# Kernel optimization log

Measured on AMD Instinct MI355X. Metric: run time of the kernel, lower is better.

The kernel has to match this reference:

```python
import jax, jax.numpy as jnp
import numpy as np

EPS = 1e-5
B, S, D = 4, 2048, 128
BALL_SCALE = 0.05  # keeps points inside the unit Poincare ball for c=1


def setup_inputs() -> dict:
    key = jax.random.key(0)
    kq, kk, kv = jax.random.split(key, 3)
    q = jax.random.normal(kq, (B, S, D), dtype=jnp.float32) * BALL_SCALE
    k = jax.random.normal(kk, (B, S, D), dtype=jnp.float32) * BALL_SCALE
    v_tangent = jax.random.normal(kv, (B, S, D), dtype=jnp.float32)
    c = jnp.asarray(1.0, dtype=jnp.float32)
    beta = jnp.asarray(0.0, dtype=jnp.float32)            # nn.Parameter init 0.0
    attention_bias = jnp.asarray(0.0, dtype=jnp.float32)  # nn.Parameter init 0.0
    return {"q": q, "k": k, "v_tangent": v_tangent, "c": c,
            "beta": beta, "attention_bias": attention_bias}


def reference(q, k, v_tangent, c, beta, attention_bias):
    sqrt_c = jnp.sqrt(c)

    # --- pairwise Poincare distance (all fp32, as in the torch autocast block) ---
    x_norm_sq = jnp.sum(q * q, axis=-1, keepdims=True)            # (B,S,1)
    y_norm_sq = jnp.sum(k * k, axis=-1, keepdims=True)            # (B,S,1)
    xy_dot = jnp.einsum('bsd,btd->bst', q, k)                     # (B,S,S)
    y_norm_sq_t = jnp.swapaxes(y_norm_sq, -2, -1)                 # (B,1,S)
    diff_norm_sq = x_norm_sq - 2.0 * xy_dot + y_norm_sq_t         # ||x-y||^2, (B,S,S)
    denom = (1.0 - c * x_norm_sq) * (1.0 - c * y_norm_sq_t)       # (B,S,S)
    arg = 1.0 + 2.0 * c * diff_norm_sq / jnp.maximum(denom, EPS)
    dist = jnp.arccosh(jnp.maximum(arg, 1.0 + EPS)) / sqrt_c      # (B,S,S)

    # --- attention ---
    beta_positive = jax.nn.softplus(beta)
    attention_scores = -beta_positive * dist - attention_bias
    attention_weights = jax.nn.softmax(attention_scores, axis=-1)  # (B,S,S)
    output_tangent = jnp.einsum('bst,btd->bsd', attention_weights, v_tangent)

    # --- exp map at origin ---
    v_norm = jnp.maximum(
        jnp.sqrt(jnp.sum(output_tangent * output_tangent, axis=-1, keepdims=True)), EPS)
    output_hyperbolic = (jnp.tanh(sqrt_c * v_norm) / sqrt_c) * (output_tangent / v_norm)

    return output_hyperbolic, attention_weights
```

## Files before the change

kernel.cpp:

```cpp
#include <hip/hip_runtime.h>
#include <math.h>

#define B_ 4
#define S_ 2048
#define D_ 128
#define EPSF 1e-5f
#define BN 128
#define PSB 272
#define PRS 4128

typedef __attribute__((ext_vector_type(8))) short short8;
typedef __attribute__((ext_vector_type(4))) float f32x4;

static __device__ __forceinline__ unsigned short f2bf(float f) {
    unsigned u = __float_as_uint(f);
    return (unsigned short)((u + 0x7fffu + ((u >> 16) & 1u)) >> 16);
}


__global__ __launch_bounds__(256) void convqk_kernel(const float* __restrict__ q,
                                                     const float* __restrict__ k,
                                                     const float* __restrict__ cp,
                                                     float* __restrict__ qn, float* __restrict__ kn,
                                                     float* __restrict__ lws,
                                                     float2* __restrict__ qng, float2* __restrict__ kng,
                                                     unsigned* __restrict__ Qb, unsigned* __restrict__ Kb) {
    int row = blockIdx.x * 4 + (threadIdx.x >> 6);
    int lane = threadIdx.x & 63;
    const int NR = B_ * S_;
    const float cc = cp[0];
    bool isQ = row < NR;
    int r = isQ ? row : row - NR;
    float2 v = ((const float2*)(isQ ? q : k))[(size_t)r * 64 + lane];
    unsigned pk = (unsigned)f2bf(v.x) | ((unsigned)f2bf(v.y) << 16);
    float nrm = v.x * v.x + v.y * v.y;
#pragma unroll
    for (int m = 1; m <= 32; m <<= 1) nrm += __shfl_xor(nrm, m, 64);
    if (isQ) {
        Qb[(size_t)r * 64 + lane] = pk;
        if (lane == 0) {
            qn[r] = nrm;
            qng[r] = make_float2(nrm, 2.f * cc * __builtin_amdgcn_rcpf(1.f - cc * nrm));
        }
        if (lane == 1) lws[r] = 0.f;
    } else {
        int b = r >> 11, rbk = r & 2047;
        int tile = rbk >> 7, n = rbk & 127;
        Kb[(size_t)b * 131072 + tile * 8192 + (lane >> 4) * 2048 + n * 16 +
           ((lane >> 2) & 3) * 4 + (lane & 3)] = pk;
        if (lane == 0) {
            kn[r] = nrm;
            kng[r] = make_float2(nrm, __builtin_amdgcn_rcpf(1.f - cc * nrm));
        }
    }
}

__global__ __launch_bounds__(256) void convv_kernel(const float* __restrict__ v, uint4* __restrict__ Vtb) {
    __shared__ unsigned short Vs[128 * 132];
    int b = blockIdx.x >> 4;
    int t = blockIdx.x & 15;
    int tid = threadIdx.x;
    const float* src = v + ((size_t)b * S_ + t * 128) * D_;
    int d4 = tid & 31, key0 = tid >> 5;
#pragma unroll
    for (int it = 0; it < 16; ++it) {
        int key = key0 + it * 8;
        float4 f = *(const float4*)(src + (size_t)key * D_ + d4 * 4);
        unsigned short* dst = &Vs[key * 132 + d4 * 4];
        dst[0] = f2bf(f.x); dst[1] = f2bf(f.y); dst[2] = f2bf(f.z); dst[3] = f2bf(f.w);
    }
    __syncthreads();
    uint4* tile = Vtb + (size_t)blockIdx.x * (128 * 16);
    int d = tid & 127;
    int cl = tid >> 7;
#pragma unroll
    for (int it = 0; it < 8; ++it) {
        int c = cl + it * 2;
        int kb = c * 8;
        unsigned short e0 = Vs[(kb + 0) * 132 + d], e1 = Vs[(kb + 1) * 132 + d];
        unsigned short e2 = Vs[(kb + 2) * 132 + d], e3 = Vs[(kb + 3) * 132 + d];
        unsigned short e4 = Vs[(kb + 4) * 132 + d], e5 = Vs[(kb + 5) * 132 + d];
        unsigned short e6 = Vs[(kb + 6) * 132 + d], e7 = Vs[(kb + 7) * 132 + d];
        uint4 o;
        o.x = (unsigned)e0 | ((unsigned)e1 << 16);
        o.y = (unsigned)e2 | ((unsigned)e3 << 16);
        o.z = (unsigned)e4 | ((unsigned)e5 << 16);
        o.w = (unsigned)e6 | ((unsigned)e7 << 16);
        tile[(c >> 2) * 512 + d * 4 + (c & 3)] = o;
    }
}


__global__ __launch_bounds__(512, 4) void hattn8_kernel(
    const unsigned short* __restrict__ Qb, const char* __restrict__ Kb, const char* __restrict__ Vtb,
    const float2* __restrict__ qng, const float2* __restrict__ kng,
    const float* __restrict__ cp, const float* __restrict__ betap, const float* __restrict__ biasp,
    float* __restrict__ hout, float* __restrict__ wout) {

    __shared__ __align__(1024) char smem[66304];
    float* l_row = (float*)(smem + 66176);
    float* nsq_s = (float*)(smem + 66240);

    const int tid = threadIdx.x;
    const int lane = tid & 63, wave = tid >> 6;
    const int wn = wave;
    const int lm = lane & 15, quad = lane >> 4;

    int xcd = blockIdx.x & 7;
    int b = xcd >> 1;
    int rb = (blockIdx.x >> 3) * 2 + (xcd & 1);
    int s0 = rb * 16;
    const size_t bS = (size_t)b * S_;

    const float beta = betap[0], bias = biasp[0];
    const float cc = cp[0];
    const float beta_pos = fmaxf(beta, 0.f) + log1pf(__expf(-fabsf(beta)));
    const float sqrt_c = sqrtf(cc);
    const float bneg = -beta_pos / sqrt_c;
    const float bias2 = -bias * 1.442695040888963f;
    const float onepe = 1.f + EPSF;

    const char* KbBase = Kb + (size_t)b * 524288;
    const char* VtBase = Vtb + (size_t)b * 16 * 32768;

    if (tid < 16) {
        float2 x = qng[bS + s0 + tid];
        *(float2*)(smem + 66048 + tid * 8) = x;
    } else if (tid < 32) {
        l_row[tid - 16] = 0.f;
    } else if (tid < 48) {
        nsq_s[tid - 32] = 0.f;
    }

    const int n0 = wn * 16 + lm;
    const int foff = n0 * 64 + quad * 16;
    short8 kf[4];
    float2 yg;
    {
#pragma unroll
        for (int ks = 0; ks < 4; ++ks)
            kf[ks] = *(const short8*)(KbBase + ks * 8192 + foff);
        yg = kng[bS + n0];
    }

    short8 aq[4];
    {
        const unsigned short* qrow = Qb + (bS + s0 + lm) * D_;
#pragma unroll
        for (int ks = 0; ks < 4; ++ks)
            aq[ks] = *(const short8*)(qrow + ks * 32 + quad * 8);
    }

    __syncthreads();

    float2 xr4[4];
#pragma unroll
    for (int r = 0; r < 4; ++r)
        xr4[r] = *(const float2*)(smem + 66048 + (quad * 4 + r) * 8);

    f32x4 o = {0.f, 0.f, 0.f, 0.f};
    float lacc[4] = {0.f, 0.f, 0.f, 0.f};

    for (int it = 0; it < 16; ++it) {
        short8 kfn[4], vf[4];
        float2 ygn;
        {
            const char* vb = VtBase + (size_t)it * 32768 + foff;
#pragma unroll
            for (int ks = 0; ks < 4; ++ks)
                vf[ks] = *(const short8*)(vb + ks * 8192);
        }
        if (it < 15) {
            const char* kb = KbBase + (size_t)(it + 1) * 32768 + foff;
#pragma unroll
            for (int ks = 0; ks < 4; ++ks)
                kfn[ks] = *(const short8*)(kb + ks * 8192);
            ygn = kng[bS + (size_t)(it + 1) * 128 + n0];
        }
        __builtin_amdgcn_sched_barrier(0);

        f32x4 acc = {0.f, 0.f, 0.f, 0.f};
#pragma unroll
        for (int ks = 0; ks < 4; ++ks)
            acc = __builtin_amdgcn_mfma_f32_16x16x32_bf16(aq[ks], kf[ks], acc, 0, 0, 0);

#pragma unroll
        for (int r = 0; r < 4; ++r) {
            int row = quad * 4 + r;
            float diff = fmaf(-2.f, acc[r], xr4[r].x + yg.x);
            float arg = fmaf(diff * yg.y, xr4[r].y, 1.f);
            arg = fmaxf(arg, onepe);
            float w = arg + sqrtf(fmaf(arg, arg, -1.f));
            float pv = __builtin_amdgcn_exp2f(fmaf(bneg, __builtin_amdgcn_logf(w), bias2));
            *(unsigned short*)(smem + row * PRS + (it * 128 + n0) * 2) = f2bf(pv);
            lacc[r] += pv;
        }
        __syncthreads();

        {
            const char* prow = smem + lm * PRS + it * 256 + quad * 16;
#pragma unroll
            for (int ks = 0; ks < 4; ++ks) {
                short8 ap = *(const short8*)(prow + ks * 64);
                o = __builtin_amdgcn_mfma_f32_16x16x32_bf16(ap, vf[ks], o, 0, 0, 0);
            }
        }

        if (it < 15) {
#pragma unroll
            for (int ks = 0; ks < 4; ++ks) kf[ks] = kfn[ks];
            yg = ygn;
        }
    }

#pragma unroll
    for (int r = 0; r < 4; ++r) {
        float s = lacc[r];
#pragma unroll
        for (int m = 1; m <= 8; m <<= 1) s += __shfl_xor(s, m, 64);
        if (lm == 0) atomicAdd(&l_row[quad * 4 + r], s);
    }
    __syncthreads();

    float linv[4];
#pragma unroll
    for (int r = 0; r < 4; ++r) linv[r] = 1.f / l_row[quad * 4 + r];

#pragma unroll
    for (int r = 0; r < 4; ++r) {
        float x = o[r] * linv[r];
        o[r] = x;
        float np = x * x;
#pragma unroll
        for (int m = 1; m <= 8; m <<= 1) np += __shfl_xor(np, m, 64);
        if (lm == 0) atomicAdd(&nsq_s[quad * 4 + r], np);
    }
    __syncthreads();
#pragma unroll
    for (int r = 0; r < 4; ++r) {
        int row = quad * 4 + r;
        float vn = fmaxf(sqrtf(nsq_s[row]), EPSF);
        float a = sqrt_c * vn;
        float th = 1.f - 2.f / (__expf(2.f * a) + 1.f);
        float sc = th / a;
        hout[(bS + s0 + row) * D_ + n0] = o[r] * sc;
    }

    {
        float4* wdst = (float4*)(wout + (bS + s0) * (size_t)S_);
#pragma unroll
        for (int j = 0; j < 8; ++j) {
            int idx = tid + j * 512;
            int row = idx >> 8;
            int ch = idx & 255;
            float lr = 1.f / l_row[row];
            uint4 u = *(const uint4*)(smem + row * PRS + ch * 16);
            float4 f0, f1;
            f0.x = __uint_as_float(u.x << 16) * lr;
            f0.y = __uint_as_float(u.x & 0xffff0000u) * lr;
            f0.z = __uint_as_float(u.y << 16) * lr;
            f0.w = __uint_as_float(u.y & 0xffff0000u) * lr;
            f1.x = __uint_as_float(u.z << 16) * lr;
            f1.y = __uint_as_float(u.z & 0xffff0000u) * lr;
            f1.z = __uint_as_float(u.w << 16) * lr;
            f1.w = __uint_as_float(u.w & 0xffff0000u) * lr;
            wdst[idx * 2] = f0;
            wdst[idx * 2 + 1] = f1;
        }
    }
}


__global__ __launch_bounds__(512, 2) void hattn_kernel(
    const unsigned short* __restrict__ Qb, const char* __restrict__ Kb, const char* __restrict__ Vtb,
    const float* __restrict__ qn, const float* __restrict__ kn,
    const float* __restrict__ cp, const float* __restrict__ betap, const float* __restrict__ biasp,
    float* __restrict__ lws, float* __restrict__ houtg, float* __restrict__ woutg) {

    __shared__ __align__(1024) char smem[75136];
    char* KsB = smem;
    char* VtB = smem + 32768;
    char* PsB = smem + 65536;
    float* kn_s  = (float*)(smem + 74240);
    float* qn_s  = (float*)(smem + 74752);
    float* l_row = (float*)(smem + 74880);
    float* nsq_s = (float*)(smem + 75008);

    const int tid = threadIdx.x;
    const int lane = tid & 63, wave = tid >> 6;
    const int wm = wave & 1, wn = wave >> 1;
    const int lm = lane & 15, quad = lane >> 4;

    int xcd = blockIdx.x & 7;
    int b = xcd >> 1;
    int rb = (blockIdx.x >> 3) * 2 + (xcd & 1);
    int s0 = rb * 32;
    const size_t bS = (size_t)b * S_;

    const float cc = cp[0], beta = betap[0], bias = biasp[0];
    const float beta_pos = fmaxf(beta, 0.f) + log1pf(__expf(-fabsf(beta)));
    const float sqrt_c = sqrtf(cc);
    const float inv_sqrt_c = 1.f / sqrt_c;

    if (tid < 32) {
        qn_s[tid] = qn[bS + s0 + tid];
        l_row[tid] = 0.f;
        nsq_s[tid] = 0.f;
    }

    short8 aq[4];
    {
        const unsigned short* qrow = Qb + (bS + s0 + wm * 16 + lm) * D_;
#pragma unroll
        for (int ks = 0; ks < 4; ++ks)
            aq[ks] = *(const short8*)(qrow + ks * 32 + quad * 8);
    }

    f32x4 o0 = {0.f, 0.f, 0.f, 0.f}, o1 = {0.f, 0.f, 0.f, 0.f};

    const char* KbBase = Kb + (size_t)b * 524288;
    const char* VtBase = Vtb + (size_t)b * 16 * 32768;

    for (int t = 0; t < S_ / BN; ++t) {
        int t0 = t * BN;
        __syncthreads();
        {
            const uint4* ksrc = (const uint4*)(KbBase + (size_t)t * 32768);
            const uint4* vsrc = (const uint4*)(VtBase + (size_t)t * 32768);
            uint4* kd = (uint4*)KsB;
            uint4* vd = (uint4*)VtB;
#pragma unroll
            for (int i = 0; i < 4; ++i) {
                kd[tid + i * 512] = ksrc[tid + i * 512];
                vd[tid + i * 512] = vsrc[tid + i * 512];
            }
            if (tid < BN) kn_s[tid] = kn[bS + t0 + tid];
        }
        __syncthreads();

        int n0 = wn * 32 + lm;
        f32x4 acc0 = {0.f, 0.f, 0.f, 0.f}, acc1 = {0.f, 0.f, 0.f, 0.f};
#pragma unroll
        for (int ks = 0; ks < 4; ++ks) {
            short8 b0 = *(const short8*)(KsB + ks * 8192 + n0 * 64 + quad * 16);
            short8 b1 = *(const short8*)(KsB + ks * 8192 + (n0 + 16) * 64 + quad * 16);
            acc0 = __builtin_amdgcn_mfma_f32_16x16x32_bf16(aq[ks], b0, acc0, 0, 0, 0);
            acc1 = __builtin_amdgcn_mfma_f32_16x16x32_bf16(aq[ks], b1, acc1, 0, 0, 0);
        }

        float lp[4];
#pragma unroll
        for (int r = 0; r < 4; ++r) {
            int row = wm * 16 + quad * 4 + r;
            float xn = qn_s[row];
            float fx = 1.f - cc * xn;
            float p0, p1;
#pragma unroll
            for (int nt = 0; nt < 2; ++nt) {
                int col = wn * 32 + nt * 16 + lm;
                float dot = (nt == 0) ? acc0[r] : acc1[r];
                float yn = kn_s[col];
                float diff = xn - 2.f * dot + yn;
                float den = fmaxf(fx * (1.f - cc * yn), EPSF);
                float arg = fmaf(2.f * cc * diff, __builtin_amdgcn_rcpf(den), 1.f);
                arg = fmaxf(arg, 1.f + EPSF);
                float dist = __logf(arg + sqrtf(arg * arg - 1.f)) * inv_sqrt_c;
                float p = __expf(fmaf(-beta_pos, dist, -bias));
                woutg[(bS + s0 + row) * S_ + t0 + col] = p;
                *(unsigned short*)(PsB + row * PSB + col * 2) = f2bf(p);
                if (nt == 0) p0 = p; else p1 = p;
            }
            lp[r] = p0 + p1;
        }
#pragma unroll
        for (int r = 0; r < 4; ++r) {
            float s = lp[r];
#pragma unroll
            for (int m = 1; m <= 8; m <<= 1) s += __shfl_xor(s, m, 64);
            if (lm == 0) atomicAdd(&l_row[wm * 16 + quad * 4 + r], s);
        }
        __syncthreads();

#pragma unroll
        for (int ks = 0; ks < 4; ++ks) {
            short8 ap = *(const short8*)(PsB + (wm * 16 + lm) * PSB + (ks * 32 + quad * 8) * 2);
            int d0 = wn * 32 + lm;
            short8 v0 = *(const short8*)(VtB + ks * 8192 + d0 * 64 + quad * 16);
            short8 v1 = *(const short8*)(VtB + ks * 8192 + (d0 + 16) * 64 + quad * 16);
            o0 = __builtin_amdgcn_mfma_f32_16x16x32_bf16(ap, v0, o0, 0, 0, 0);
            o1 = __builtin_amdgcn_mfma_f32_16x16x32_bf16(ap, v1, o1, 0, 0, 0);
        }
    }
    __syncthreads();

    float xs0[4], xs1[4];
#pragma unroll
    for (int r = 0; r < 4; ++r) {
        int row = wm * 16 + quad * 4 + r;
        float linv = __builtin_amdgcn_rcpf(l_row[row]);
        float x0 = o0[r] * linv, x1 = o1[r] * linv;
        xs0[r] = x0; xs1[r] = x1;
        float np = x0 * x0 + x1 * x1;
#pragma unroll
        for (int m = 1; m <= 8; m <<= 1) np += __shfl_xor(np, m, 64);
        if (lm == 0) atomicAdd(&nsq_s[row], np);
    }
    if (tid < 32) lws[bS + s0 + tid] = l_row[tid];
    __syncthreads();
#pragma unroll
    for (int r = 0; r < 4; ++r) {
        int row = wm * 16 + quad * 4 + r;
        float vn = fmaxf(sqrtf(nsq_s[row]), EPSF);
        float a = sqrt_c * vn;
        float th = 1.f - 2.f * __builtin_amdgcn_rcpf(__expf(2.f * a) + 1.f);
        float sc = th / a;
        houtg[(bS + s0 + row) * D_ + wn * 32 + lm] = xs0[r] * sc;
        houtg[(bS + s0 + row) * D_ + wn * 32 + 16 + lm] = xs1[r] * sc;
    }
}

__global__ __launch_bounds__(256) void wnorm_kernel(float* __restrict__ w,
                                                    const float* __restrict__ lws) {
    size_t idx = (size_t)blockIdx.x * 256 + threadIdx.x;
    int row = (int)(idx >> 9);
    float linv = 1.f / lws[row];
    float4* p = (float4*)w + idx;
    float4 v = *p;
    v.x *= linv; v.y *= linv; v.z *= linv; v.w *= linv;
    *p = v;
}


extern "C" void kernel_launch(void* const* d_in, const int* in_sizes, int n_in,
                              void* d_out, int out_size, void* d_ws, size_t ws_size,
                              hipStream_t stream) {
    const float* q    = (const float*)d_in[0];
    const float* k    = (const float*)d_in[1];
    const float* v    = (const float*)d_in[2];
    const float* c    = (const float*)d_in[3];
    const float* beta = (const float*)d_in[4];
    const float* ab   = (const float*)d_in[5];

    float* out  = (float*)d_out;
    float* hout = out;
    float* wout = out + (size_t)B_ * S_ * D_;

    float* qn  = (float*)d_ws;
    float* kn  = qn + B_ * S_;
    float* lws = kn + B_ * S_;
    char*  wsb = (char*)d_ws;
    const size_t QG_OFF = 98304;
    const size_t KG_OFF = QG_OFF + 65536;
    const size_t QB_OFF = KG_OFF + 65536;
    const size_t KB_OFF = QB_OFF + 2097152;
    const size_t VT_OFF = KB_OFF + 2097152;
    const size_t NEED1  = VT_OFF + 2097152;

    float2*  qng = (float2*)(wsb + QG_OFF);
    float2*  kng = (float2*)(wsb + KG_OFF);
    unsigned* Qb = (unsigned*)(wsb + QB_OFF);
    unsigned* Kb = (unsigned*)(wsb + KB_OFF);
    uint4*   Vtb = (uint4*)(wsb + VT_OFF);

    if (ws_size >= NEED1) {
        convqk_kernel<<<4096, 256, 0, stream>>>(q, k, c, qn, kn, lws, qng, kng, Qb, Kb);
        convv_kernel<<<64, 256, 0, stream>>>(v, Vtb);
        hattn8_kernel<<<512, 512, 0, stream>>>((const unsigned short*)Qb, (const char*)Kb,
                                               (const char*)Vtb, qng, kng, c, beta, ab,
                                               hout, wout);
    } else {
        convqk_kernel<<<4096, 256, 0, stream>>>(q, k, c, qn, kn, lws, qng, kng, Qb, Kb);
        convv_kernel<<<64, 256, 0, stream>>>(v, Vtb);
        hattn_kernel<<<256, 512, 0, stream>>>((const unsigned short*)Qb, (const char*)Kb,
                                              (const char*)Vtb, qn, kn, c, beta, ab,
                                              lws, hout, wout);
        wnorm_kernel<<<(B_ * S_ * S_ / 4) / 256, 256, 0, stream>>>(wout, lws);
    }
}
```

Baseline: 137.8 us.

## Split keys across waves with register-shuffled P and LDS output reduction

The main attention kernel changes from each wave owning a 16-key column slice per tile, with a block-wide barrier every iteration, to each wave owning its own 32-key chunks. It computes S transposed (keys × queries) so the probabilities can be reshuffled in registers into the A operand of the PV MFMA, feeding eight output accumulators across all 128 value dims. Per-wave partial outputs are then reduced through LDS atomics before normalization and the exp map. This removes the per-iteration __syncthreads and the LDS round trip for P, but adds register pressure, cross-wave atomic reductions and extra LDS. K is now stored row-major, and the fallback kernel gains an XOR swizzle to match.

```diff
diff --git a/kernel.cpp b/kernel.cpp
--- a/kernel.cpp
+++ b/kernel.cpp
@@ -44,10 +44,7 @@
         }
         if (lane == 1) lws[r] = 0.f;
     } else {
-        int b = r >> 11, rbk = r & 2047;
-        int tile = rbk >> 7, n = rbk & 127;
-        Kb[(size_t)b * 131072 + tile * 8192 + (lane >> 4) * 2048 + n * 16 +
-           ((lane >> 2) & 3) * 4 + (lane & 3)] = pk;
+        Kb[(size_t)r * 64 + lane] = pk;
         if (lane == 0) {
             kn[r] = nrm;
             kng[r] = make_float2(nrm, __builtin_amdgcn_rcpf(1.f - cc * nrm));
@@ -91,19 +88,20 @@
 }
 
 
-__global__ __launch_bounds__(512, 4) void hattn8_kernel(
-    const unsigned short* __restrict__ Qb, const char* __restrict__ Kb, const char* __restrict__ Vtb,
+__global__ __launch_bounds__(512, 4) void hattn9_kernel(
+    const unsigned short* __restrict__ Qb, const unsigned short* __restrict__ Kb,
+    const char* __restrict__ Vtb,
     const float2* __restrict__ qng, const float2* __restrict__ kng,
     const float* __restrict__ cp, const float* __restrict__ betap, const float* __restrict__ biasp,
     float* __restrict__ hout, float* __restrict__ wout) {
 
-    __shared__ __align__(1024) char smem[66304];
-    float* l_row = (float*)(smem + 66176);
-    float* nsq_s = (float*)(smem + 66240);
+    __shared__ __align__(1024) char smem[74368];
+    float* O_red = (float*)(smem + 66048);
+    float* l_row = (float*)(smem + 74240);
+    float* nsq_s = (float*)(smem + 74304);
 
     const int tid = threadIdx.x;
-    const int lane = tid & 63, wave = tid >> 6;
-    const int wn = wave;
+    const int lane = tid & 63, wn = tid >> 6;
     const int lm = lane & 15, quad = lane >> 4;
 
     int xcd = blockIdx.x & 7;
@@ -120,28 +118,15 @@
     const float bias2 = -bias * 1.442695040888963f;
     const float onepe = 1.f + EPSF;
 
-    const char* KbBase = Kb + (size_t)b * 524288;
+    const unsigned short* KbR = Kb + bS * D_;
     const char* VtBase = Vtb + (size_t)b * 16 * 32768;
 
-    if (tid < 16) {
-        float2 x = qng[bS + s0 + tid];
-        *(float2*)(smem + 66048 + tid * 8) = x;
-    } else if (tid < 32) {
-        l_row[tid - 16] = 0.f;
-    } else if (tid < 48) {
-        nsq_s[tid - 32] = 0.f;
-    }
-
-    const int n0 = wn * 16 + lm;
-    const int foff = n0 * 64 + quad * 16;
-    short8 kf[4];
-    float2 yg;
-    {
-#pragma unroll
-        for (int ks = 0; ks < 4; ++ks)
-            kf[ks] = *(const short8*)(KbBase + ks * 8192 + foff);
-        yg = kng[bS + n0];
-    }
+#pragma unroll
+    for (int j = 0; j < 4; ++j) O_red[tid + j * 512] = 0.f;
+    if (tid < 16) l_row[tid] = 0.f;
+    else if (tid < 32) nsq_s[tid - 16] = 0.f;
+
+    const float2 xq = qng[bS + s0 + lm];
 
     short8 aq[4];
     {
@@ -150,100 +135,148 @@
         for (int ks = 0; ks < 4; ++ks)
             aq[ks] = *(const short8*)(qrow + ks * 32 + quad * 8);
     }
-
     __syncthreads();
 
-    float2 xr4[4];
-#pragma unroll
-    for (int r = 0; r < 4; ++r)
-        xr4[r] = *(const float2*)(smem + 66048 + (quad * 4 + r) * 8);
-
-    f32x4 o = {0.f, 0.f, 0.f, 0.f};
-    float lacc[4] = {0.f, 0.f, 0.f, 0.f};
-
-    for (int it = 0; it < 16; ++it) {
-        short8 kfn[4], vf[4];
-        float2 ygn;
-        {
-            const char* vb = VtBase + (size_t)it * 32768 + foff;
-#pragma unroll
-            for (int ks = 0; ks < 4; ++ks)
-                vf[ks] = *(const short8*)(vb + ks * 8192);
-        }
-        if (it < 15) {
-            const char* kb = KbBase + (size_t)(it + 1) * 32768 + foff;
-#pragma unroll
-            for (int ks = 0; ks < 4; ++ks)
-                kfn[ks] = *(const short8*)(kb + ks * 8192);
-            ygn = kng[bS + (size_t)(it + 1) * 128 + n0];
-        }
-        __builtin_amdgcn_sched_barrier(0);
-
-        f32x4 acc = {0.f, 0.f, 0.f, 0.f};
-#pragma unroll
-        for (int ks = 0; ks < 4; ++ks)
-            acc = __builtin_amdgcn_mfma_f32_16x16x32_bf16(aq[ks], kf[ks], acc, 0, 0, 0);
-
+    f32x4 o0 = {0,0,0,0}, o1 = {0,0,0,0}, o2 = {0,0,0,0}, o3 = {0,0,0,0};
+    f32x4 o4 = {0,0,0,0}, o5 = {0,0,0,0}, o6 = {0,0,0,0}, o7 = {0,0,0,0};
+    float lacc = 0.f;
+
+    const int srcA = lm + ((quad & 1) << 5);
+    const int srcB = srcA + 16;
+    const bool hiT = quad >= 2;
+
+    for (int ci = 0; ci < 8; ++ci) {
+        const int chunk = ci * 8 + wn;
+        const int key0 = chunk * 32;
+
+        const unsigned short* krow = KbR + (size_t)(key0 + lm) * D_;
+        short8 kfA[4], kfB[4];
+#pragma unroll
+        for (int ks = 0; ks < 4; ++ks) {
+            kfA[ks] = *(const short8*)(krow + ks * 32 + quad * 8);
+            kfB[ks] = *(const short8*)(krow + 16 * D_ + ks * 32 + quad * 8);
+        }
+
+        float2 ygA[4], ygB[4];
 #pragma unroll
         for (int r = 0; r < 4; ++r) {
-            int row = quad * 4 + r;
-            float diff = fmaf(-2.f, acc[r], xr4[r].x + yg.x);
-            float arg = fmaf(diff * yg.y, xr4[r].y, 1.f);
-            arg = fmaxf(arg, onepe);
+            ygA[r] = kng[bS + key0 + quad * 4 + r];
+            ygB[r] = kng[bS + key0 + 16 + quad * 4 + r];
+        }
+
+        f32x4 sA = {0,0,0,0}, sB = {0,0,0,0};
+#pragma unroll
+        for (int ks = 0; ks < 4; ++ks) {
+            sA = __builtin_amdgcn_mfma_f32_16x16x32_bf16(kfA[ks], aq[ks], sA, 0, 0, 0);
+            sB = __builtin_amdgcn_mfma_f32_16x16x32_bf16(kfB[ks], aq[ks], sB, 0, 0, 0);
+        }
+
+        unsigned short pb[8];
+#pragma unroll
+        for (int r = 0; r < 4; ++r) {
+            float diff = fmaf(-2.f, sA[r], xq.x + ygA[r].x);
+            float arg = fmaxf(fmaf(diff * ygA[r].y, xq.y, 1.f), onepe);
             float w = arg + sqrtf(fmaf(arg, arg, -1.f));
             float pv = __builtin_amdgcn_exp2f(fmaf(bneg, __builtin_amdgcn_logf(w), bias2));
-            *(unsigned short*)(smem + row * PRS + (it * 128 + n0) * 2) = f2bf(pv);
-            lacc[r] += pv;
-        }
-        __syncthreads();
+            pb[r] = f2bf(pv);
+            lacc += pv;
+
+            float diff2 = fmaf(-2.f, sB[r], xq.x + ygB[r].x);
+            float arg2 = fmaxf(fmaf(diff2 * ygB[r].y, xq.y, 1.f), onepe);
+            float w2 = arg2 + sqrtf(fmaf(arg2, arg2, -1.f));
+            float pv2 = __builtin_amdgcn_exp2f(fmaf(bneg, __builtin_amdgcn_logf(w2), bias2));
+            pb[4 + r] = f2bf(pv2);
+            lacc += pv2;
+        }
+        unsigned u0 = (unsigned)pb[0] | ((unsigned)pb[1] << 16);
+        unsigned u1 = (unsigned)pb[2] | ((unsigned)pb[3] << 16);
+        unsigned u2 = (unsigned)pb[4] | ((unsigned)pb[5] << 16);
+        unsigned u3 = (unsigned)pb[6] | ((unsigned)pb[7] << 16);
 
         {
-            const char* prow = smem + lm * PRS + it * 256 + quad * 16;
-#pragma unroll
-            for (int ks = 0; ks < 4; ++ks) {
-                short8 ap = *(const short8*)(prow + ks * 64);
-                o = __builtin_amdgcn_mfma_f32_16x16x32_bf16(ap, vf[ks], o, 0, 0, 0);
-            }
-        }
-
-        if (it < 15) {
-#pragma unroll
-            for (int ks = 0; ks < 4; ++ks) kf[ks] = kfn[ks];
-            yg = ygn;
-        }
-    }
-
-#pragma unroll
-    for (int r = 0; r < 4; ++r) {
-        float s = lacc[r];
-#pragma unroll
-        for (int m = 1; m <= 8; m <<= 1) s += __shfl_xor(s, m, 64);
-        if (lm == 0) atomicAdd(&l_row[quad * 4 + r], s);
+            char* pw = smem + lm * PRS + (key0 + quad * 4) * 2;
+            *(uint2*)pw = make_uint2(u0, u1);
+            *(uint2*)(pw + 32) = make_uint2(u2, u3);
+        }
+
+        unsigned a0, a1, a2, a3;
+        {
+            unsigned f0 = __shfl((int)u0, srcA), f1 = __shfl((int)u1, srcA);
+            unsigned f2 = __shfl((int)u0, srcB), f3 = __shfl((int)u1, srcB);
+            unsigned g0 = __shfl((int)u2, srcA), g1 = __shfl((int)u3, srcA);
+            unsigned g2 = __shfl((int)u2, srcB), g3 = __shfl((int)u3, srcB);
+            a0 = hiT ? g0 : f0; a1 = hiT ? g1 : f1;
+            a2 = hiT ? g2 : f2; a3 = hiT ? g3 : f3;
+        }
+        union { unsigned u[4]; short8 s; } pa;
+        pa.u[0] = a0; pa.u[1] = a1; pa.u[2] = a2; pa.u[3] = a3;
+
+        const char* vb = VtBase + (size_t)(chunk >> 2) * 32768 + (chunk & 3) * 8192
+                         + lm * 64 + quad * 16;
+        {
+            short8 vf;
+            vf = *(const short8*)(vb + 0 * 1024);
+            o0 = __builtin_amdgcn_mfma_f32_16x16x32_bf16(pa.s, vf, o0, 0, 0, 0);
+            vf = *(const short8*)(vb + 1 * 1024);
+            o1 = __builtin_amdgcn_mfma_f32_16x16x32_bf16(pa.s, vf, o1, 0, 0, 0);
+            vf = *(const short8*)(vb + 2 * 1024);
+            o2 = __builtin_amdgcn_mfma_f32_16x16x32_bf16(pa.s, vf, o2, 0, 0, 0);
+            vf = *(const short8*)(vb + 3 * 1024);
+            o3 = __builtin_amdgcn_mfma_f32_16x16x32_bf16(pa.s, vf, o3, 0, 0, 0);
+            vf = *(const short8*)(vb + 4 * 1024);
+            o4 = __builtin_amdgcn_mfma_f32_16x16x32_bf16(pa.s, vf, o4, 0, 0, 0);
+            vf = *(const short8*)(vb + 5 * 1024);
+            o5 = __builtin_amdgcn_mfma_f32_16x16x32_bf16(pa.s, vf, o5, 0, 0, 0);
+            vf = *(const short8*)(vb + 6 * 1024);
+            o6 = __builtin_amdgcn_mfma_f32_16x16x32_bf16(pa.s, vf, o6, 0, 0, 0);
+            vf = *(const short8*)(vb + 7 * 1024);
+            o7 = __builtin_amdgcn_mfma_f32_16x16x32_bf16(pa.s, vf, o7, 0, 0, 0);
+        }
+    }
+
+    lacc += __shfl_xor(lacc, 16, 64);
+    lacc += __shfl_xor(lacc, 32, 64);
+    if (lane < 16) atomicAdd(&l_row[lm], lacc);
+
+    {
+        float* Obase = O_red + (quad * 4) * 128 + lm;
+#pragma unroll
+        for (int r = 0; r < 4; ++r) {
+            atomicAdd(Obase + r * 128 + 0 * 16, o0[r]);
+            atomicAdd(Obase + r * 128 + 1 * 16, o1[r]);
+            atomicAdd(Obase + r * 128 + 2 * 16, o2[r]);
+            atomicAdd(Obase + r * 128 + 3 * 16, o3[r]);
+            atomicAdd(Obase + r * 128 + 4 * 16, o4[r]);
+            atomicAdd(Obase + r * 128 + 5 * 16, o5[r]);
+            atomicAdd(Obase + r * 128 + 6 * 16, o6[r]);
+            atomicAdd(Obase + r * 128 + 7 * 16, o7[r]);
+        }
     }
     __syncthreads();
 
-    float linv[4];
-#pragma unroll
-    for (int r = 0; r < 4; ++r) linv[r] = 1.f / l_row[quad * 4 + r];
-
-#pragma unroll
-    for (int r = 0; r < 4; ++r) {
-        float x = o[r] * linv[r];
-        o[r] = x;
+    float xs[4];
+#pragma unroll
+    for (int j = 0; j < 4; ++j) {
+        int idx = tid + j * 512;
+        int row = idx >> 7;
+        float x = O_red[idx] / l_row[row];
+        xs[j] = x;
         float np = x * x;
 #pragma unroll
-        for (int m = 1; m <= 8; m <<= 1) np += __shfl_xor(np, m, 64);
-        if (lm == 0) atomicAdd(&nsq_s[quad * 4 + r], np);
+        for (int m = 1; m <= 32; m <<= 1) np += __shfl_xor(np, m, 64);
+        if (lane == 0) atomicAdd(&nsq_s[row], np);
     }
     __syncthreads();
-#pragma unroll
-    for (int r = 0; r < 4; ++r) {
-        int row = quad * 4 + r;
+
+#pragma unroll
+    for (int j = 0; j < 4; ++j) {
+        int idx = tid + j * 512;
+        int row = idx >> 7;
         float vn = fmaxf(sqrtf(nsq_s[row]), EPSF);
         float a = sqrt_c * vn;
         float th = 1.f - 2.f / (__expf(2.f * a) + 1.f);
         float sc = th / a;
-        hout[(bS + s0 + row) * D_ + n0] = o[r] * sc;
+        hout[(bS + s0 + row) * D_ + (idx & 127)] = xs[j] * sc;
     }
 
     {
@@ -272,7 +305,8 @@
 
 
 __global__ __launch_bounds__(512, 2) void hattn_kernel(
-    const unsigned short* __restrict__ Qb, const char* __restrict__ Kb, const char* __restrict__ Vtb,
+    const unsigned short* __restrict__ Qb, const unsigned short* __restrict__ Kb,
+    const char* __restrict__ Vtb,
     const float* __restrict__ qn, const float* __restrict__ kn,
     const float* __restrict__ cp, const float* __restrict__ betap, const float* __restrict__ biasp,
     float* __restrict__ lws, float* __restrict__ houtg, float* __restrict__ woutg) {
@@ -318,21 +352,23 @@
 
     f32x4 o0 = {0.f, 0.f, 0.f, 0.f}, o1 = {0.f, 0.f, 0.f, 0.f};
 
-    const char* KbBase = Kb + (size_t)b * 524288;
+    const uint4* KbBase = (const uint4*)(Kb + bS * D_);
     const char* VtBase = Vtb + (size_t)b * 16 * 32768;
 
     for (int t = 0; t < S_ / BN; ++t) {
         int t0 = t * BN;
         __syncthreads();
         {
-            const uint4* ksrc = (const uint4*)(KbBase + (size_t)t * 32768);
+            const uint4* ksrc = KbBase + (size_t)t0 * 16;
             const uint4* vsrc = (const uint4*)(VtBase + (size_t)t * 32768);
             uint4* kd = (uint4*)KsB;
             uint4* vd = (uint4*)VtB;
 #pragma unroll
             for (int i = 0; i < 4; ++i) {
-                kd[tid + i * 512] = ksrc[tid + i * 512];
-                vd[tid + i * 512] = vsrc[tid + i * 512];
+                int idx = tid + i * 512;
+                int row = idx >> 4, cch = idx & 15;
+                kd[row * 16 + (cch ^ (row & 7))] = ksrc[idx];
+                vd[idx] = vsrc[idx];
             }
             if (tid < BN) kn_s[tid] = kn[bS + t0 + tid];
         }
@@ -342,8 +378,10 @@
         f32x4 acc0 = {0.f, 0.f, 0.f, 0.f}, acc1 = {0.f, 0.f, 0.f, 0.f};
 #pragma unroll
         for (int ks = 0; ks < 4; ++ks) {
-            short8 b0 = *(const short8*)(KsB + ks * 8192 + n0 * 64 + quad * 16);
-            short8 b1 = *(const short8*)(KsB + ks * 8192 + (n0 + 16) * 64 + quad * 16);
+            int c = ks * 4 + quad;
+            short8 b0 = *(const short8*)(KsB + n0 * 256 + ((c ^ (n0 & 7)) * 16));
+            int n1 = n0 + 16;
+            short8 b1 = *(const short8*)(KsB + n1 * 256 + ((c ^ (n1 & 7)) * 16));
             acc0 = __builtin_amdgcn_mfma_f32_16x16x32_bf16(aq[ks], b0, acc0, 0, 0, 0);
             acc1 = __builtin_amdgcn_mfma_f32_16x16x32_bf16(aq[ks], b1, acc1, 0, 0, 0);
         }
@@ -465,13 +503,13 @@
     if (ws_size >= NEED1) {
         convqk_kernel<<<4096, 256, 0, stream>>>(q, k, c, qn, kn, lws, qng, kng, Qb, Kb);
         convv_kernel<<<64, 256, 0, stream>>>(v, Vtb);
-        hattn8_kernel<<<512, 512, 0, stream>>>((const unsigned short*)Qb, (const char*)Kb,
+        hattn9_kernel<<<512, 512, 0, stream>>>((const unsigned short*)Qb, (const unsigned short*)Kb,
                                                (const char*)Vtb, qng, kng, c, beta, ab,
                                                hout, wout);
     } else {
         convqk_kernel<<<4096, 256, 0, stream>>>(q, k, c, qn, kn, lws, qng, kng, Qb, Kb);
         convv_kernel<<<64, 256, 0, stream>>>(v, Vtb);
-        hattn_kernel<<<256, 512, 0, stream>>>((const unsigned short*)Qb, (const char*)Kb,
+        hattn_kernel<<<256, 512, 0, stream>>>((const unsigned short*)Qb, (const unsigned short*)Kb,
                                               (const char*)Vtb, qn, kn, c, beta, ab,
                                               lws, hout, wout);
         wnorm_kernel<<<(B_ * S_ * S_ / 4) / 256, 256, 0, stream>>>(wout, lws);
```

New measurement: 190.5 us. 1.38x slower.

## Use two-pass softmax with recomputed scores to shrink LDS and stream weights

Applied to the files above, without the earlier changes.

Replaces the single-pass attention kernel, which kept a full 16x2048 bf16 probability row block in LDS, with a two-pass scheme. The first pass computes only row sums. The second pass recomputes the distance scores with the normalization folded into the exponent, then writes the normalized weights directly to global memory and uses a small double-buffered LDS tile for the PV MFMA. K gets a new transposed per-16-key layout so the score MFMA runs K-major, and the fallback kernel switches to row-major K with an XOR swizzle. The aim is far less LDS per block and higher occupancy (launch bounds raised to 6). The cost is doubling the QK matmul and transcendental work, plus an extra K layout pass in the conversion kernel.

```diff
diff --git a/kernel.cpp b/kernel.cpp
--- a/kernel.cpp
+++ b/kernel.cpp
@@ -7,7 +7,7 @@
 #define EPSF 1e-5f
 #define BN 128
 #define PSB 272
-#define PRS 4128
+#define SRS 272
 
 typedef __attribute__((ext_vector_type(8))) short short8;
 typedef __attribute__((ext_vector_type(4))) float f32x4;
@@ -24,7 +24,8 @@
                                                      float* __restrict__ qn, float* __restrict__ kn,
                                                      float* __restrict__ lws,
                                                      float2* __restrict__ qng, float2* __restrict__ kng,
-                                                     unsigned* __restrict__ Qb, unsigned* __restrict__ Kb) {
+                                                     unsigned* __restrict__ Qb, unsigned* __restrict__ Kb,
+                                                     unsigned* __restrict__ KbA) {
     int row = blockIdx.x * 4 + (threadIdx.x >> 6);
     int lane = threadIdx.x & 63;
     const int NR = B_ * S_;
@@ -44,10 +45,11 @@
         }
         if (lane == 1) lws[r] = 0.f;
     } else {
-        int b = r >> 11, rbk = r & 2047;
-        int tile = rbk >> 7, n = rbk & 127;
-        Kb[(size_t)b * 131072 + tile * 8192 + (lane >> 4) * 2048 + n * 16 +
-           ((lane >> 2) & 3) * 4 + (lane & 3)] = pk;
+        Kb[(size_t)r * 64 + lane] = pk;
+        int b = r >> 11, rloc = r & 2047;
+        int t16 = rloc >> 4, kit = rloc & 15;
+        KbA[(size_t)b * 131072 + t16 * 1024 + (lane >> 4) * 256 + kit * 16 +
+            ((lane >> 2) & 3) * 4 + (lane & 3)] = pk;
         if (lane == 0) {
             kn[r] = nrm;
             kng[r] = make_float2(nrm, __builtin_amdgcn_rcpf(1.f - cc * nrm));
@@ -91,19 +93,19 @@
 }
 
 
-__global__ __launch_bounds__(512, 4) void hattn8_kernel(
-    const unsigned short* __restrict__ Qb, const char* __restrict__ Kb, const char* __restrict__ Vtb,
+__global__ __launch_bounds__(512, 6) void hattn10_kernel(
+    const unsigned short* __restrict__ Qb, const char* __restrict__ KbA,
+    const char* __restrict__ Vtb,
     const float2* __restrict__ qng, const float2* __restrict__ kng,
     const float* __restrict__ cp, const float* __restrict__ betap, const float* __restrict__ biasp,
     float* __restrict__ hout, float* __restrict__ wout) {
 
-    __shared__ __align__(1024) char smem[66304];
-    float* l_row = (float*)(smem + 66176);
-    float* nsq_s = (float*)(smem + 66240);
+    __shared__ __align__(1024) char smem[8832];
+    float* l_row = (float*)(smem + 8704);
+    float* nsq_s = (float*)(smem + 8768);
 
     const int tid = threadIdx.x;
-    const int lane = tid & 63, wave = tid >> 6;
-    const int wn = wave;
+    const int lane = tid & 63, wn = tid >> 6;
     const int lm = lane & 15, quad = lane >> 4;
 
     int xcd = blockIdx.x & 7;
@@ -120,28 +122,13 @@
     const float bias2 = -bias * 1.442695040888963f;
     const float onepe = 1.f + EPSF;
 
-    const char* KbBase = Kb + (size_t)b * 524288;
-    const char* VtBase = Vtb + (size_t)b * 16 * 32768;
-
-    if (tid < 16) {
-        float2 x = qng[bS + s0 + tid];
-        *(float2*)(smem + 66048 + tid * 8) = x;
-    } else if (tid < 32) {
-        l_row[tid - 16] = 0.f;
-    } else if (tid < 48) {
-        nsq_s[tid - 32] = 0.f;
-    }
-
-    const int n0 = wn * 16 + lm;
-    const int foff = n0 * 64 + quad * 16;
-    short8 kf[4];
-    float2 yg;
-    {
-#pragma unroll
-        for (int ks = 0; ks < 4; ++ks)
-            kf[ks] = *(const short8*)(KbBase + ks * 8192 + foff);
-        yg = kng[bS + n0];
-    }
+    const char* KA = KbA + (size_t)b * 524288;
+    const char* Vt = Vtb + (size_t)b * 524288;
+
+    if (tid < 16) l_row[tid] = 0.f;
+    else if (tid < 32) nsq_s[tid - 16] = 0.f;
+
+    const float2 xq = qng[bS + s0 + lm];
 
     short8 aq[4];
     {
@@ -150,92 +137,107 @@
         for (int ks = 0; ks < 4; ++ks)
             aq[ks] = *(const short8*)(qrow + ks * 32 + quad * 8);
     }
-
-    __syncthreads();
-
-    float2 xr4[4];
-#pragma unroll
-    for (int r = 0; r < 4; ++r)
-        xr4[r] = *(const float2*)(smem + 66048 + (quad * 4 + r) * 8);
+    __syncthreads();
+
+    float lacc = 0.f;
+    for (int it = 0; it < 16; ++it) {
+        int t16 = it * 8 + wn;
+        const char* ka = KA + t16 * 4096 + lm * 64 + quad * 16;
+        short8 k0 = *(const short8*)(ka);
+        short8 k1 = *(const short8*)(ka + 1024);
+        short8 k2 = *(const short8*)(ka + 2048);
+        short8 k3 = *(const short8*)(ka + 3072);
+        const float4* yp = (const float4*)(kng + bS + t16 * 16 + quad * 4);
+        float4 y01 = yp[0], y23 = yp[1];
+
+        f32x4 s = {0.f, 0.f, 0.f, 0.f};
+        s = __builtin_amdgcn_mfma_f32_16x16x32_bf16(k0, aq[0], s, 0, 0, 0);
+        s = __builtin_amdgcn_mfma_f32_16x16x32_bf16(k1, aq[1], s, 0, 0, 0);
+        s = __builtin_amdgcn_mfma_f32_16x16x32_bf16(k2, aq[2], s, 0, 0, 0);
+        s = __builtin_amdgcn_mfma_f32_16x16x32_bf16(k3, aq[3], s, 0, 0, 0);
+
+        float yn[4] = {y01.x, y01.z, y23.x, y23.z};
+        float gy[4] = {y01.y, y01.w, y23.y, y23.w};
+#pragma unroll
+        for (int r = 0; r < 4; ++r) {
+            float diff = fmaf(-2.f, s[r], xq.x + yn[r]);
+            float arg = fmaxf(fmaf(diff * gy[r], xq.y, 1.f), onepe);
+            float w = arg + sqrtf(fmaf(arg, arg, -1.f));
+            lacc += __builtin_amdgcn_exp2f(fmaf(bneg, __builtin_amdgcn_logf(w), bias2));
+        }
+    }
+    lacc += __shfl_xor(lacc, 16, 64);
+    lacc += __shfl_xor(lacc, 32, 64);
+    if (lane < 16) atomicAdd(&l_row[lm], lacc);
+    __syncthreads();
+
+    const float lrow = l_row[lm];
+    const float linv = 1.f / lrow;
+    const float bias3 = bias2 - __builtin_amdgcn_logf(lrow);
 
     f32x4 o = {0.f, 0.f, 0.f, 0.f};
-    float lacc[4] = {0.f, 0.f, 0.f, 0.f};
-
+    int pbuf = 0;
     for (int it = 0; it < 16; ++it) {
-        short8 kfn[4], vf[4];
-        float2 ygn;
+        int t16 = it * 8 + wn;
+        const char* ka = KA + t16 * 4096 + lm * 64 + quad * 16;
+        short8 k0 = *(const short8*)(ka);
+        short8 k1 = *(const short8*)(ka + 1024);
+        short8 k2 = *(const short8*)(ka + 2048);
+        short8 k3 = *(const short8*)(ka + 3072);
+        const float4* yp = (const float4*)(kng + bS + t16 * 16 + quad * 4);
+        float4 y01 = yp[0], y23 = yp[1];
+
+        f32x4 s = {0.f, 0.f, 0.f, 0.f};
+        s = __builtin_amdgcn_mfma_f32_16x16x32_bf16(k0, aq[0], s, 0, 0, 0);
+        s = __builtin_amdgcn_mfma_f32_16x16x32_bf16(k1, aq[1], s, 0, 0, 0);
+        s = __builtin_amdgcn_mfma_f32_16x16x32_bf16(k2, aq[2], s, 0, 0, 0);
+        s = __builtin_amdgcn_mfma_f32_16x16x32_bf16(k3, aq[3], s, 0, 0, 0);
+
+        float yn[4] = {y01.x, y01.z, y23.x, y23.z};
+        float gy[4] = {y01.y, y01.w, y23.y, y23.w};
+        float pv[4];
+#pragma unroll
+        for (int r = 0; r < 4; ++r) {
+            float diff = fmaf(-2.f, s[r], xq.x + yn[r]);
+            float arg = fmaxf(fmaf(diff * gy[r], xq.y, 1.f), onepe);
+            float w = arg + sqrtf(fmaf(arg, arg, -1.f));
+            pv[r] = __builtin_amdgcn_exp2f(fmaf(bneg, __builtin_amdgcn_logf(w), bias3));
+        }
+
         {
-            const char* vb = VtBase + (size_t)it * 32768 + foff;
-#pragma unroll
-            for (int ks = 0; ks < 4; ++ks)
-                vf[ks] = *(const short8*)(vb + ks * 8192);
-        }
-        if (it < 15) {
-            const char* kb = KbBase + (size_t)(it + 1) * 32768 + foff;
-#pragma unroll
-            for (int ks = 0; ks < 4; ++ks)
-                kfn[ks] = *(const short8*)(kb + ks * 8192);
-            ygn = kng[bS + (size_t)(it + 1) * 128 + n0];
-        }
-        __builtin_amdgcn_sched_barrier(0);
-
-        f32x4 acc = {0.f, 0.f, 0.f, 0.f};
-#pragma unroll
-        for (int ks = 0; ks < 4; ++ks)
-            acc = __builtin_amdgcn_mfma_f32_16x16x32_bf16(aq[ks], kf[ks], acc, 0, 0, 0);
-
-#pragma unroll
-        for (int r = 0; r < 4; ++r) {
-            int row = quad * 4 + r;
-            float diff = fmaf(-2.f, acc[r], xr4[r].x + yg.x);
-            float arg = fmaf(diff * yg.y, xr4[r].y, 1.f);
-            arg = fmaxf(arg, onepe);
-            float w = arg + sqrtf(fmaf(arg, arg, -1.f));
-            float pv = __builtin_amdgcn_exp2f(fmaf(bneg, __builtin_amdgcn_logf(w), bias2));
-            *(unsigned short*)(smem + row * PRS + (it * 128 + n0) * 2) = f2bf(pv);
-            lacc[r] += pv;
+            float4 wv = {pv[0], pv[1], pv[2], pv[3]};
+            *(float4*)(wout + (bS + s0 + lm) * (size_t)S_ + t16 * 16 + quad * 4) = wv;
+        }
+
+        {
+            unsigned u0 = (unsigned)f2bf(pv[0]) | ((unsigned)f2bf(pv[1]) << 16);
+            unsigned u1 = (unsigned)f2bf(pv[2]) | ((unsigned)f2bf(pv[3]) << 16);
+            *(uint2*)(smem + pbuf * 4352 + lm * SRS + wn * 32 + quad * 8) = make_uint2(u0, u1);
         }
         __syncthreads();
 
         {
-            const char* prow = smem + lm * PRS + it * 256 + quad * 16;
-#pragma unroll
-            for (int ks = 0; ks < 4; ++ks) {
-                short8 ap = *(const short8*)(prow + ks * 64);
-                o = __builtin_amdgcn_mfma_f32_16x16x32_bf16(ap, vf[ks], o, 0, 0, 0);
+            const char* sr = smem + pbuf * 4352 + lm * SRS;
+            const char* vb = Vt + (size_t)it * 32768 + (wn * 16 + lm) * 64 + quad * 16;
+#pragma unroll
+            for (int kq = 0; kq < 4; ++kq) {
+                short8 ap = *(const short8*)(sr + kq * 64 + quad * 16);
+                short8 vf = *(const short8*)(vb + kq * 8192);
+                o = __builtin_amdgcn_mfma_f32_16x16x32_bf16(ap, vf, o, 0, 0, 0);
             }
         }
-
-        if (it < 15) {
-#pragma unroll
-            for (int ks = 0; ks < 4; ++ks) kf[ks] = kfn[ks];
-            yg = ygn;
-        }
+        pbuf ^= 1;
     }
 
 #pragma unroll
     for (int r = 0; r < 4; ++r) {
-        float s = lacc[r];
-#pragma unroll
-        for (int m = 1; m <= 8; m <<= 1) s += __shfl_xor(s, m, 64);
-        if (lm == 0) atomicAdd(&l_row[quad * 4 + r], s);
-    }
-    __syncthreads();
-
-    float linv[4];
-#pragma unroll
-    for (int r = 0; r < 4; ++r) linv[r] = 1.f / l_row[quad * 4 + r];
-
-#pragma unroll
-    for (int r = 0; r < 4; ++r) {
-        float x = o[r] * linv[r];
-        o[r] = x;
-        float np = x * x;
+        float np = o[r] * o[r];
 #pragma unroll
         for (int m = 1; m <= 8; m <<= 1) np += __shfl_xor(np, m, 64);
         if (lm == 0) atomicAdd(&nsq_s[quad * 4 + r], np);
     }
     __syncthreads();
+
 #pragma unroll
     for (int r = 0; r < 4; ++r) {
         int row = quad * 4 + r;
@@ -243,36 +245,14 @@
         float a = sqrt_c * vn;
         float th = 1.f - 2.f / (__expf(2.f * a) + 1.f);
         float sc = th / a;
-        hout[(bS + s0 + row) * D_ + n0] = o[r] * sc;
-    }
-
-    {
-        float4* wdst = (float4*)(wout + (bS + s0) * (size_t)S_);
-#pragma unroll
-        for (int j = 0; j < 8; ++j) {
-            int idx = tid + j * 512;
-            int row = idx >> 8;
-            int ch = idx & 255;
-            float lr = 1.f / l_row[row];
-            uint4 u = *(const uint4*)(smem + row * PRS + ch * 16);
-            float4 f0, f1;
-            f0.x = __uint_as_float(u.x << 16) * lr;
-            f0.y = __uint_as_float(u.x & 0xffff0000u) * lr;
-            f0.z = __uint_as_float(u.y << 16) * lr;
-            f0.w = __uint_as_float(u.y & 0xffff0000u) * lr;
-            f1.x = __uint_as_float(u.z << 16) * lr;
-            f1.y = __uint_as_float(u.z & 0xffff0000u) * lr;
-            f1.z = __uint_as_float(u.w << 16) * lr;
-            f1.w = __uint_as_float(u.w & 0xffff0000u) * lr;
-            wdst[idx * 2] = f0;
-            wdst[idx * 2 + 1] = f1;
-        }
+        hout[(bS + s0 + row) * D_ + wn * 16 + lm] = o[r] * sc;
     }
 }
 
 
 __global__ __launch_bounds__(512, 2) void hattn_kernel(
-    const unsigned short* __restrict__ Qb, const char* __restrict__ Kb, const char* __restrict__ Vtb,
+    const unsigned short* __restrict__ Qb, const unsigned short* __restrict__ Kb,
+    const char* __restrict__ Vtb,
     const float* __restrict__ qn, const float* __restrict__ kn,
     const float* __restrict__ cp, const float* __restrict__ betap, const float* __restrict__ biasp,
     float* __restrict__ lws, float* __restrict__ houtg, float* __restrict__ woutg) {
@@ -318,21 +298,23 @@
 
     f32x4 o0 = {0.f, 0.f, 0.f, 0.f}, o1 = {0.f, 0.f, 0.f, 0.f};
 
-    const char* KbBase = Kb + (size_t)b * 524288;
+    const uint4* KbBase = (const uint4*)(Kb + bS * D_);
     const char* VtBase = Vtb + (size_t)b * 16 * 32768;
 
     for (int t = 0; t < S_ / BN; ++t) {
         int t0 = t * BN;
         __syncthreads();
         {
-            const uint4* ksrc = (const uint4*)(KbBase + (size_t)t * 32768);
+            const uint4* ksrc = KbBase + (size_t)t0 * 16;
             const uint4* vsrc = (const uint4*)(VtBase + (size_t)t * 32768);
             uint4* kd = (uint4*)KsB;
             uint4* vd = (uint4*)VtB;
 #pragma unroll
             for (int i = 0; i < 4; ++i) {
-                kd[tid + i * 512] = ksrc[tid + i * 512];
-                vd[tid + i * 512] = vsrc[tid + i * 512];
+                int idx = tid + i * 512;
+                int row = idx >> 4, cch = idx & 15;
+                kd[row * 16 + (cch ^ (row & 7))] = ksrc[idx];
+                vd[idx] = vsrc[idx];
             }
             if (tid < BN) kn_s[tid] = kn[bS + t0 + tid];
         }
@@ -342,8 +324,10 @@
         f32x4 acc0 = {0.f, 0.f, 0.f, 0.f}, acc1 = {0.f, 0.f, 0.f, 0.f};
 #pragma unroll
         for (int ks = 0; ks < 4; ++ks) {
-            short8 b0 = *(const short8*)(KsB + ks * 8192 + n0 * 64 + quad * 16);
-            short8 b1 = *(const short8*)(KsB + ks * 8192 + (n0 + 16) * 64 + quad * 16);
+            int c = ks * 4 + quad;
+            short8 b0 = *(const short8*)(KsB + n0 * 256 + ((c ^ (n0 & 7)) * 16));
+            int n1 = n0 + 16;
+            short8 b1 = *(const short8*)(KsB + n1 * 256 + ((c ^ (n1 & 7)) * 16));
             acc0 = __builtin_amdgcn_mfma_f32_16x16x32_bf16(aq[ks], b0, acc0, 0, 0, 0);
             acc1 = __builtin_amdgcn_mfma_f32_16x16x32_bf16(aq[ks], b1, acc1, 0, 0, 0);
         }
@@ -454,24 +438,26 @@
     const size_t QB_OFF = KG_OFF + 65536;
     const size_t KB_OFF = QB_OFF + 2097152;
     const size_t VT_OFF = KB_OFF + 2097152;
-    const size_t NEED1  = VT_OFF + 2097152;
+    const size_t KA_OFF = VT_OFF + 2097152;
+    const size_t NEED1  = KA_OFF + 2097152;
 
     float2*  qng = (float2*)(wsb + QG_OFF);
     float2*  kng = (float2*)(wsb + KG_OFF);
     unsigned* Qb = (unsigned*)(wsb + QB_OFF);
     unsigned* Kb = (unsigned*)(wsb + KB_OFF);
     uint4*   Vtb = (uint4*)(wsb + VT_OFF);
+    unsigned* KbA = (unsigned*)(wsb + KA_OFF);
 
     if (ws_size >= NEED1) {
-        convqk_kernel<<<4096, 256, 0, stream>>>(q, k, c, qn, kn, lws, qng, kng, Qb, Kb);
+        convqk_kernel<<<4096, 256, 0, stream>>>(q, k, c, qn, kn, lws, qng, kng, Qb, Kb, KbA);
         convv_kernel<<<64, 256, 0, stream>>>(v, Vtb);
-        hattn8_kernel<<<512, 512, 0, stream>>>((const unsigned short*)Qb, (const char*)Kb,
-                                               (const char*)Vtb, qng, kng, c, beta, ab,
-                                               hout, wout);
+        hattn10_kernel<<<512, 512, 0, stream>>>((const unsigned short*)Qb, (const char*)KbA,
+                                                (const char*)Vtb, qng, kng, c, beta, ab,
+                                                hout, wout);
     } else {
-        convqk_kernel<<<4096, 256, 0, stream>>>(q, k, c, qn, kn, lws, qng, kng, Qb, Kb);
+        convqk_kernel<<<4096, 256, 0, stream>>>(q, k, c, qn, kn, lws, qng, kng, Qb, Kb, KbA);
         convv_kernel<<<64, 256, 0, stream>>>(v, Vtb);
-        hattn_kernel<<<256, 512, 0, stream>>>((const unsigned short*)Qb, (const char*)Kb,
+        hattn_kernel<<<256, 512, 0, stream>>>((const unsigned short*)Qb, (const unsigned short*)Kb,
                                               (const char*)Vtb, qn, kn, c, beta, ab,
                                               lws, hout, wout);
         wnorm_kernel<<<(B_ * S_ * S_ / 4) / 256, 256, 0, stream>>>(wout, lws);
```

Result: slower. 154.6 us (+12.1%).
